# Performance work log

Hardware: AMD Instinct MI355X
Metric: run time of the kernel (lower is better)

Reference implementation:

```python
import math
import jax, jax.numpy as jnp
import numpy as np

CAPACITY_FACTOR = 1.0
MIN_CAPACITY = 4


def setup_inputs() -> dict:
    key = jax.random.key(0)
    k1, k2 = jax.random.split(key)
    x = jax.random.normal(k1, (8192, 1024), dtype=jnp.float32)
    wg = jax.random.normal(k2, (1024, 64), dtype=jnp.float32) * 0.02
    return {"x": x, "wg": wg}


def reference(x, wg):
    # Gate projection: [S, D] @ [D, E] -> [S, E]
    logits = x @ wg
    S, E = logits.shape
    # _capacity: ceil(S / E * capacity_factor * 2) for top-2, floored at min_capacity (static)
    capacity = max(math.ceil((S / E) * (CAPACITY_FACTOR * 2.0)), MIN_CAPACITY)

    gates = jax.nn.softmax(logits, axis=-1)           # [S, E]
    org_gates = gates

    # top-1 expert
    indices1_s = jnp.argmax(gates, axis=1)
    mask1 = jax.nn.one_hot(indices1_s, E, dtype=jnp.int32)
    # top-2 expert (deterministic: no gumbel sampling)
    logits_except1 = jnp.where(mask1.astype(bool), -jnp.inf, logits)
    indices2_s = jnp.argmax(logits_except1, axis=1)
    mask2 = jax.nn.one_hot(indices2_s, E, dtype=jnp.int32)

    # per-expert running positions
    locations1 = jnp.cumsum(mask1, axis=0) - 1        # [S, E]
    locations2 = jnp.cumsum(mask2, axis=0) - 1 + jnp.sum(mask1, axis=0, keepdims=True)

    # load-balancing aux loss
    me = jnp.mean(gates, axis=0)
    ce = jnp.mean(mask1.astype(gates.dtype), axis=0)
    l_aux = jnp.sum(me * ce) * E * E

    exp_counts = jnp.sum(mask1 + mask2, axis=0)

    # drop tokens over capacity
    mask1 = mask1 * (locations1 < capacity).astype(jnp.int32)
    mask2 = mask2 * (locations2 < capacity).astype(jnp.int32)

    locations1_s = jnp.sum(locations1 * mask1, axis=1)  # [S]
    locations2_s = jnp.sum(locations2 * mask2, axis=1)

    mask1_f = mask1.astype(gates.dtype)
    mask2_f = mask2.astype(gates.dtype)
    gates1_s = jnp.sum(gates * mask1_f, axis=1)
    gates2_s = jnp.sum(gates * mask2_f, axis=1)
    denom_s = jnp.clip(gates1_s + gates2_s, jnp.finfo(gates.dtype).eps)
    gates1_s = gates1_s / denom_s
    gates2_s = gates2_s / denom_s

    gates1 = gates1_s[:, None] * mask1_f              # [S, E]
    gates2 = gates2_s[:, None] * mask2_f

    locations1_sc = jax.nn.one_hot(locations1_s, capacity, dtype=gates.dtype)  # [S, C]
    locations2_sc = jax.nn.one_hot(locations2_s, capacity, dtype=gates.dtype)

    combine_weights = (jnp.einsum('se,sc->sec', gates1, locations1_sc)
                       + jnp.einsum('se,sc->sec', gates2, locations2_sc))  # [S, E, C]
    dispatch_mask = combine_weights.astype(bool)
    return l_aux, combine_weights, dispatch_mask, exp_counts, org_gates
```

## Files before the change

kernel.cpp:

```cpp
#include <hip/hip_runtime.h>
#include <math.h>

#define S_TOKENS 8192
#define D_DIM    1024
#define E_EXP    64
#define CAPACITY 256
#define TPB      64
#define NBLK     (S_TOKENS / TPB)
#define NZBLK    4096

typedef float fx4 __attribute__((ext_vector_type(4)));

#define SZ_COMBINE   (134217728LL)
#define OFF_COMBINE  (1LL)
#define OFF_DISPATCH (OFF_COMBINE + SZ_COMBINE)
#define OFF_EXPCNT   (OFF_DISPATCH + SZ_COMBINE)
#define OFF_ORGGATES (OFF_EXPCNT + E_EXP)

#define WS_IDX1 0
#define WS_IDX2 (WS_IDX1 + S_TOKENS)
#define WS_G1   (WS_IDX2 + S_TOKENS)
#define WS_G2   (WS_G1 + S_TOKENS)
#define WS_CNT1 (WS_G2 + S_TOKENS)
#define WS_CNT2 (WS_CNT1 + NBLK * E_EXP)
#define WS_OFF1 (WS_CNT2 + NBLK * E_EXP)
#define WS_OFF2 (WS_OFF1 + NBLK * E_EXP)
#define WS_MEP  (WS_OFF2 + NBLK * E_EXP)

__global__ __launch_bounds__(256) void k1_gemm_gate(
    const float* __restrict__ x, const float* __restrict__ wg,
    float* __restrict__ out, int* __restrict__ wsi, float* __restrict__ wsf) {
  const int bid = blockIdx.x;
  const int tid = threadIdx.x;

  if (bid >= NBLK) {
    fx4 z = (fx4)0.f;
    fx4* p = (fx4*)out;
    const size_t n4 = (size_t)(2 * SZ_COMBINE) / 4;
    const size_t nth = (size_t)NZBLK * 256;
    for (size_t i = (size_t)(bid - NBLK) * 256 + tid; i < n4; i += nth)
      __builtin_nontemporal_store(z, &p[i]);
    if (bid == NBLK && tid == 0) out[2 * SZ_COMBINE] = 0.0f;
    return;
  }

  __shared__ float xs[64][68];
  __shared__ float ovl[64 * 68];
  __shared__ float mM[64], rS[64];
  __shared__ int   li1[64], li2[64];
  __shared__ float mered[16][64];

  float (*wsh)[64] = (float(*)[64])ovl;
  float (*Lg)[68]  = (float(*)[68])ovl;

  const int tx = tid & 15;
  const int ty = tid >> 4;
  const int s0 = bid * TPB;

  float acc[4][4];
#pragma unroll
  for (int i = 0; i < 4; i++)
#pragma unroll
    for (int q = 0; q < 4; q++) acc[i][q] = 0.f;

  for (int k0 = 0; k0 < D_DIM; k0 += 64) {
#pragma unroll
    for (int r = 0; r < 4; r++) {
      int i = tid + 256 * r;
      int t = i >> 4, c = i & 15;
      *(fx4*)&xs[t][4 * c] =
          *(const fx4*)&x[(size_t)(s0 + t) * D_DIM + k0 + 4 * c];
      *(fx4*)&wsh[t][4 * c] =
          *(const fx4*)&wg[(size_t)(k0 + t) * E_EXP + 4 * c];
    }
    __syncthreads();
    for (int kb = 0; kb < 64; kb += 4) {
      fx4 xa[4], wb[4];
#pragma unroll
      for (int i = 0; i < 4; i++) xa[i] = *(fx4*)&xs[ty + 16 * i][kb];
#pragma unroll
      for (int j = 0; j < 4; j++) wb[j] = *(fx4*)&wsh[kb + j][4 * tx];
#pragma unroll
      for (int j = 0; j < 4; j++)
#pragma unroll
        for (int i = 0; i < 4; i++) {
          float xv = xa[i][j];
#pragma unroll
          for (int q = 0; q < 4; q++)
            acc[i][q] = fmaf(xv, wb[j][q], acc[i][q]);
        }
    }
    __syncthreads();
  }

#pragma unroll
  for (int i = 0; i < 4; i++) {
    fx4 v;
#pragma unroll
    for (int q = 0; q < 4; q++) v[q] = acc[i][q];
    *(fx4*)&Lg[ty + 16 * i][4 * tx] = v;
  }
  __syncthreads();

  {
    const int g = tid >> 2;
    const int u = tid & 3;
    float bv = -INFINITY; int bi = 0;
#pragma unroll
    for (int i = 0; i < 16; i++) {
      int ee = u + 4 * i;
      float v = Lg[g][ee];
      if (v > bv) { bv = v; bi = ee; }
    }
#pragma unroll
    for (int d = 1; d < 4; d <<= 1) {
      float ovv = __shfl_xor(bv, d, 4);
      int   oi  = __shfl_xor(bi, d, 4);
      if (ovv > bv || (ovv == bv && oi < bi)) { bv = ovv; bi = oi; }
    }
    const float m1 = bv; const int i1 = bi;

    float se = 0.f;
#pragma unroll
    for (int i = 0; i < 16; i++) se += expf(Lg[g][u + 4 * i] - m1);
#pragma unroll
    for (int d = 1; d < 4; d <<= 1) se += __shfl_xor(se, d, 4);

    float bv2 = -INFINITY; int bi2 = 0;
#pragma unroll
    for (int i = 0; i < 16; i++) {
      int ee = u + 4 * i;
      float v = Lg[g][ee];
      if (ee != i1 && v > bv2) { bv2 = v; bi2 = ee; }
    }
#pragma unroll
    for (int d = 1; d < 4; d <<= 1) {
      float ovv = __shfl_xor(bv2, d, 4);
      int   oi  = __shfl_xor(bi2, d, 4);
      if (ovv > bv2 || (ovv == bv2 && oi < bi2)) { bv2 = ovv; bi2 = oi; }
    }

    if (u == 0) {
      float rs = 1.0f / se;
      mM[g] = m1; rS[g] = rs;
      li1[g] = i1; li2[g] = bi2;
      int s = s0 + g;
      wsi[WS_IDX1 + s] = i1;
      wsi[WS_IDX2 + s] = bi2;
      wsf[WS_G1 + s] = rs;
      wsf[WS_G2 + s] = expf(bv2 - m1) * rs;
    }
  }
  __syncthreads();

  {
    float ms[4] = {0.f, 0.f, 0.f, 0.f};
#pragma unroll
    for (int i = 0; i < 4; i++) {
      int t = ty + 16 * i;
      float m = mM[t], r = rS[t];
      size_t ob = OFF_ORGGATES + (size_t)(s0 + t) * E_EXP + 4 * tx;
#pragma unroll
      for (int q = 0; q < 4; q++) {
        float gate = expf(Lg[t][4 * tx + q] - m) * r;
        out[ob + q] = gate;
        ms[q] += gate;
      }
    }
#pragma unroll
    for (int q = 0; q < 4; q++) mered[ty][4 * tx + q] = ms[q];
  }
  __syncthreads();

  if (tid < 64) {
    float s = 0.f;
#pragma unroll
    for (int yy = 0; yy < 16; yy++) s += mered[yy][tid];
    wsf[WS_MEP + bid * 64 + tid] = s;
    int c1 = 0, c2 = 0;
    for (int t = 0; t < TPB; t++) {
      c1 += (li1[t] == tid);
      c2 += (li2[t] == tid);
    }
    wsi[WS_CNT1 + bid * 64 + tid] = c1;
    wsi[WS_CNT2 + bid * 64 + tid] = c2;
  }
}

__global__ __launch_bounds__(1024) void k2_scan(
    float* __restrict__ out, int* __restrict__ wsi, float* __restrict__ wsf) {
  __shared__ int lc[NBLK * E_EXP];
  __shared__ float mep[16][E_EXP];
  __shared__ int tot1[E_EXP];

  const int tid = threadIdx.x;

  {
    const int e = tid & 63, cg = tid >> 6;
    float s = 0.f;
#pragma unroll
    for (int c = cg * 8; c < cg * 8 + 8; c++) s += wsf[WS_MEP + c * 64 + e];
    mep[cg][e] = s;
  }

  {
    const int4* g = (const int4*)&wsi[WS_CNT1];
    int4* l = (int4*)lc;
#pragma unroll
    for (int i = tid; i < NBLK * E_EXP / 4; i += 1024) l[i] = g[i];
  }
  __syncthreads();

  if (tid < E_EXP) {
    int run = 0;
#pragma unroll 8
    for (int c = 0; c < NBLK; c++) {
      wsi[WS_OFF1 + c * 64 + tid] = run;
      run += lc[c * 64 + tid];
    }
    tot1[tid] = run;
  }
  __syncthreads();

  {
    const int4* g = (const int4*)&wsi[WS_CNT2];
    int4* l = (int4*)lc;
#pragma unroll
    for (int i = tid; i < NBLK * E_EXP / 4; i += 1024) l[i] = g[i];
  }
  __syncthreads();

  if (tid < E_EXP) {
    const int e = tid;
    const int total1 = tot1[e];
    int run = total1;
#pragma unroll 8
    for (int c = 0; c < NBLK; c++) {
      wsi[WS_OFF2 + c * 64 + e] = run;
      run += lc[c * 64 + e];
    }
    const int total2 = run - total1;

    out[OFF_EXPCNT + e] = (float)(total1 + total2);

    float mesum = 0.f;
#pragma unroll
    for (int cg = 0; cg < 16; cg++) mesum += mep[cg][e];
    float me = mesum * (1.0f / 8192.0f);
    float ce = (float)total1 * (1.0f / 8192.0f);
    float prod = me * ce * 4096.0f;
#pragma unroll
    for (int d = 1; d < 64; d <<= 1) prod += __shfl_xor(prod, d, 64);
    if (e == 0) out[0] = prod;
  }
}

__global__ __launch_bounds__(64) void k3_scatter(
    float* __restrict__ out, const int* __restrict__ wsi,
    const float* __restrict__ wsf) {
  __shared__ int li1[TPB], li2[TPB];
  const int bid = blockIdx.x;
  const int t = threadIdx.x;
  const int s0 = bid * TPB;

  li1[t] = wsi[WS_IDX1 + s0 + t];
  li2[t] = wsi[WS_IDX2 + s0 + t];
  __syncthreads();

  const int e1 = li1[t], e2 = li2[t];
  int r1 = 0, r2 = 0;
  for (int j = 0; j < t; j++) {
    r1 += (li1[j] == e1);
    r2 += (li2[j] == e2);
  }
  const int loc1 = wsi[WS_OFF1 + bid * 64 + e1] + r1;
  const int loc2 = wsi[WS_OFF2 + bid * 64 + e2] + r2;
  const int s = s0 + t;

  const float g1r = wsf[WS_G1 + s];
  const float g2r = wsf[WS_G2 + s];
  const bool d1 = (loc1 >= CAPACITY);
  const bool d2 = (loc2 >= CAPACITY);
  const float g1f = d1 ? 0.f : g1r;
  const float g2f = d2 ? 0.f : g2r;
  const float denom = fmaxf(g1f + g2f, 1.1920929e-7f);
  const float w1 = g1f / denom;
  const float w2 = g2f / denom;

  if (!d1) {
    size_t o = OFF_COMBINE + (size_t)s * (E_EXP * CAPACITY) +
               (size_t)e1 * CAPACITY + loc1;
    out[o] = w1;
    out[o + SZ_COMBINE] = (w1 != 0.f) ? 1.f : 0.f;
  }
  if (!d2) {
    size_t o = OFF_COMBINE + (size_t)s * (E_EXP * CAPACITY) +
               (size_t)e2 * CAPACITY + loc2;
    out[o] = w2;
    out[o + SZ_COMBINE] = (w2 != 0.f) ? 1.f : 0.f;
  }
}

extern "C" void kernel_launch(void* const* d_in, const int* in_sizes, int n_in,
                              void* d_out, int out_size, void* d_ws,
                              size_t ws_size, hipStream_t stream) {
  const float* x  = (const float*)d_in[0];
  const float* wg = (const float*)d_in[1];
  float* out = (float*)d_out;
  int*   wsi = (int*)d_ws;
  float* wsf = (float*)d_ws;

  hipLaunchKernelGGL(k1_gemm_gate, dim3(NBLK + NZBLK), dim3(256), 0, stream,
                     x, wg, out, wsi, wsf);
  hipLaunchKernelGGL(k2_scan, dim3(1), dim3(1024), 0, stream, out, wsi, wsf);
  hipLaunchKernelGGL(k3_scatter, dim3(NBLK), dim3(64), 0, stream, out, wsi,
                     wsf);
}
```

Baseline: 1.133 ms.

## Fuse scan into scatter kernel with per-block redundant prefix sums; use plain stores for zero fill

Removes the single-block scan kernel. Each scatter block now computes its own per-expert prefix offsets by summing the count arrays over preceding blocks, and one extra block computes totals, expert counts and the aux loss. This drops one launch and a serial single-block stage, at the cost of redundant reads of the count arrays by every block. The large zero fill also switches from nontemporal to regular vector stores.

```diff
diff --git a/kernel.cpp b/kernel.cpp
--- a/kernel.cpp
+++ b/kernel.cpp
@@ -23,11 +23,9 @@
 #define WS_G2   (WS_G1 + S_TOKENS)
 #define WS_CNT1 (WS_G2 + S_TOKENS)
 #define WS_CNT2 (WS_CNT1 + NBLK * E_EXP)
-#define WS_OFF1 (WS_CNT2 + NBLK * E_EXP)
-#define WS_OFF2 (WS_OFF1 + NBLK * E_EXP)
-#define WS_MEP  (WS_OFF2 + NBLK * E_EXP)
-
-__global__ __launch_bounds__(256) void k1_gemm_gate(
+#define WS_MEP  (WS_CNT2 + NBLK * E_EXP)
+
+__global__ __launch_bounds__(256) void kA_gemm_fill(
     const float* __restrict__ x, const float* __restrict__ wg,
     float* __restrict__ out, int* __restrict__ wsi, float* __restrict__ wsf) {
   const int bid = blockIdx.x;
@@ -39,7 +37,7 @@
     const size_t n4 = (size_t)(2 * SZ_COMBINE) / 4;
     const size_t nth = (size_t)NZBLK * 256;
     for (size_t i = (size_t)(bid - NBLK) * 256 + tid; i < n4; i += nth)
-      __builtin_nontemporal_store(z, &p[i]);
+      p[i] = z;
     if (bid == NBLK && tid == 0) out[2 * SZ_COMBINE] = 0.0f;
     return;
   }
@@ -187,82 +185,51 @@
   }
 }
 
-__global__ __launch_bounds__(1024) void k2_scan(
-    float* __restrict__ out, int* __restrict__ wsi, float* __restrict__ wsf) {
-  __shared__ int lc[NBLK * E_EXP];
-  __shared__ float mep[16][E_EXP];
-  __shared__ int tot1[E_EXP];
-
-  const int tid = threadIdx.x;
-
-  {
-    const int e = tid & 63, cg = tid >> 6;
-    float s = 0.f;
-#pragma unroll
-    for (int c = cg * 8; c < cg * 8 + 8; c++) s += wsf[WS_MEP + c * 64 + e];
-    mep[cg][e] = s;
-  }
-
-  {
-    const int4* g = (const int4*)&wsi[WS_CNT1];
-    int4* l = (int4*)lc;
-#pragma unroll
-    for (int i = tid; i < NBLK * E_EXP / 4; i += 1024) l[i] = g[i];
-  }
-  __syncthreads();
-
-  if (tid < E_EXP) {
-    int run = 0;
+__global__ __launch_bounds__(64) void kB_scan_scatter(
+    float* __restrict__ out, const int* __restrict__ wsi,
+    const float* __restrict__ wsf) {
+  const int bid = blockIdx.x;
+  const int e = threadIdx.x;
+
+  if (bid == NBLK) {
+    int t1 = 0, t2 = 0;
+    float ms = 0.f;
 #pragma unroll 8
     for (int c = 0; c < NBLK; c++) {
-      wsi[WS_OFF1 + c * 64 + tid] = run;
-      run += lc[c * 64 + tid];
-    }
-    tot1[tid] = run;
-  }
-  __syncthreads();
+      t1 += wsi[WS_CNT1 + c * 64 + e];
+      t2 += wsi[WS_CNT2 + c * 64 + e];
+      ms += wsf[WS_MEP + c * 64 + e];
+    }
+    out[OFF_EXPCNT + e] = (float)(t1 + t2);
+    float me = ms * (1.0f / 8192.0f);
+    float ce = (float)t1 * (1.0f / 8192.0f);
+    float prod = me * ce * 4096.0f;
+#pragma unroll
+    for (int d = 1; d < 64; d <<= 1) prod += __shfl_xor(prod, d, 64);
+    if (e == 0) out[0] = prod;
+    return;
+  }
+
+  __shared__ int soff1[64], soff2[64];
+  __shared__ int li1[TPB], li2[TPB];
 
   {
-    const int4* g = (const int4*)&wsi[WS_CNT2];
-    int4* l = (int4*)lc;
-#pragma unroll
-    for (int i = tid; i < NBLK * E_EXP / 4; i += 1024) l[i] = g[i];
-  }
-  __syncthreads();
-
-  if (tid < E_EXP) {
-    const int e = tid;
-    const int total1 = tot1[e];
-    int run = total1;
+    int o1 = 0, o2 = 0, t1 = 0;
 #pragma unroll 8
     for (int c = 0; c < NBLK; c++) {
-      wsi[WS_OFF2 + c * 64 + e] = run;
-      run += lc[c * 64 + e];
-    }
-    const int total2 = run - total1;
-
-    out[OFF_EXPCNT + e] = (float)(total1 + total2);
-
-    float mesum = 0.f;
-#pragma unroll
-    for (int cg = 0; cg < 16; cg++) mesum += mep[cg][e];
-    float me = mesum * (1.0f / 8192.0f);
-    float ce = (float)total1 * (1.0f / 8192.0f);
-    float prod = me * ce * 4096.0f;
-#pragma unroll
-    for (int d = 1; d < 64; d <<= 1) prod += __shfl_xor(prod, d, 64);
-    if (e == 0) out[0] = prod;
-  }
-}
-
-__global__ __launch_bounds__(64) void k3_scatter(
-    float* __restrict__ out, const int* __restrict__ wsi,
-    const float* __restrict__ wsf) {
-  __shared__ int li1[TPB], li2[TPB];
-  const int bid = blockIdx.x;
-  const int t = threadIdx.x;
+      int c1 = wsi[WS_CNT1 + c * 64 + e];
+      t1 += c1;
+      if (c < bid) {
+        o1 += c1;
+        o2 += wsi[WS_CNT2 + c * 64 + e];
+      }
+    }
+    soff1[e] = o1;
+    soff2[e] = t1 + o2;
+  }
+
+  const int t = e;
   const int s0 = bid * TPB;
-
   li1[t] = wsi[WS_IDX1 + s0 + t];
   li2[t] = wsi[WS_IDX2 + s0 + t];
   __syncthreads();
@@ -273,8 +240,8 @@
     r1 += (li1[j] == e1);
     r2 += (li2[j] == e2);
   }
-  const int loc1 = wsi[WS_OFF1 + bid * 64 + e1] + r1;
-  const int loc2 = wsi[WS_OFF2 + bid * 64 + e2] + r2;
+  const int loc1 = soff1[e1] + r1;
+  const int loc2 = soff2[e2] + r2;
   const int s = s0 + t;
 
   const float g1r = wsf[WS_G1 + s];
@@ -310,9 +277,8 @@
   int*   wsi = (int*)d_ws;
   float* wsf = (float*)d_ws;
 
-  hipLaunchKernelGGL(k1_gemm_gate, dim3(NBLK + NZBLK), dim3(256), 0, stream,
+  hipLaunchKernelGGL(kA_gemm_fill, dim3(NBLK + NZBLK), dim3(256), 0, stream,
                      x, wg, out, wsi, wsf);
-  hipLaunchKernelGGL(k2_scan, dim3(1), dim3(1024), 0, stream, out, wsi, wsf);
-  hipLaunchKernelGGL(k3_scatter, dim3(NBLK), dim3(64), 0, stream, out, wsi,
-                     wsf);
+  hipLaunchKernelGGL(kB_scan_scatter, dim3(NBLK + 1), dim3(64), 0, stream,
+                     out, wsi, wsf);
 }
```

Result: slower. 1.163 ms (+2.6%).
